# Kernel tuning notes

Hardware: AMD Instinct MI355X
Metric: run time of the kernel (lower is better)

The kernel has to match this reference:

```python
import jax, jax.numpy as jnp
import numpy as np

N = 1024       # nodes
D1 = 64        # hidden_dim_1
D2 = 64        # hidden_dim_2
E = 16384      # edges
P = 8192       # query pairs
MAXX = 100     # max node label -> Embedding(MAXX+1, D1)
EPS = 1e-5     # LayerNorm eps (no affine)


def _ln(t):
    m = jnp.mean(t, axis=-1, keepdims=True)
    v = jnp.mean((t - m) ** 2, axis=-1, keepdims=True)
    return (t - m) / jnp.sqrt(v + EPS)


def setup_inputs() -> dict:
    key = jax.random.key(0)
    ks = jax.random.split(key, 12)
    s = 0.1
    x = jax.random.randint(ks[0], (N,), 0, MAXX + 1)
    ei = jax.random.randint(ks[1], (2, E), 0, N)
    pos = jax.random.randint(ks[2], (P, 2), 0, N)
    emb = jax.random.normal(ks[3], (MAXX + 1, D1)) * s
    sage_Wl = jax.random.normal(ks[4], (2, D1, D1)) * s   # lin_l weight (aggr path, has bias)
    sage_bl = jnp.zeros((2, D1))
    sage_Wr = jax.random.normal(ks[5], (2, D1, D1)) * s   # lin_r weight (root path, no bias)
    h_W = jax.random.normal(ks[6], (D1 + 1, D2)) * s
    h_b = jnp.zeros((D2,))
    g_W = jax.random.normal(ks[7], (D1 + 1 + 2 * D2, D2)) * s
    g_b = jnp.zeros((D2,))
    lin_W = jax.random.normal(ks[8], (D2, 1)) * s
    lin_b = jnp.zeros((1,))
    return {"x": x, "ei": ei, "pos": pos, "emb": emb,
            "sage_Wl": sage_Wl, "sage_bl": sage_bl, "sage_Wr": sage_Wr,
            "h_W": h_W, "h_b": h_b, "g_W": g_W, "g_b": g_b,
            "lin_W": lin_W, "lin_b": lin_b}


def reference(x, ei, pos, emb, sage_Wl, sage_bl, sage_Wr, h_W, h_b, g_W, g_b, lin_W, lin_b):
    n = N
    src, dst = ei[0], ei[1]
    h = emb[x]                                            # (n, D1)
    # SAGEConv x2: mean-aggregate src->dst, lin_l(aggr)+bias + lin_r(root); then LN (no affine, no relu)
    deg = jax.ops.segment_sum(jnp.ones((E,), h.dtype), dst, num_segments=n)
    deg = jnp.maximum(deg, 1.0)[:, None]
    for i in range(2):
        aggr = jax.ops.segment_sum(h[src], dst, num_segments=n) / deg
        h = _ln(aggr @ sage_Wl[i] + sage_bl[i] + h @ sage_Wr[i])
    # pairwise outer product features: (n, n, D1)
    A = h[:, None, :] * h[None, :, :]
    eim = jnp.zeros((n * n,), h.dtype).at[src * n + dst].set(1.0).reshape(n, n, 1)
    A = jnp.concatenate([A, eim], axis=-1)                # (n, n, D1+1)
    # mataggr: B = h_1(A); row/col sums; D = cat(A, vec_p, vec_q); g_1(D)
    B = jax.nn.relu(_ln(A @ h_W + h_b))                   # (n, n, D2)
    vec_p = jnp.sum(B, axis=1, keepdims=True)             # (n, 1, D2)
    vec_q = jnp.sum(B, axis=0, keepdims=True)             # (1, n, D2)
    Dm = jnp.concatenate([A,
                          jnp.broadcast_to(vec_p, (n, n, D2)),
                          jnp.broadcast_to(vec_q, (n, n, D2))], axis=-1)
    G = jax.nn.relu(_ln(Dm @ g_W + g_b))                  # (n, n, D2)
    # symmetrize and gather query pairs
    S = (G * jnp.transpose(G, (1, 0, 2))).reshape(n * n, D2)
    sel = S[pos[:, 0] * n + pos[:, 1]]                    # (P, D2)
    return sel @ lin_W + lin_b                            # (P, 1)
```

## Files before the change

### kernel.cpp

```cpp
#include <hip/hip_runtime.h>
#include <hip/hip_bf16.h>
#include <hip/hip_cooperative_groups.h>

#define NN 1024
#define DD 64
#define EE 16384
#define PP 8192
#define EPSF 1e-5f
#define SWP (DD + 8)
#define SMEM_BYTES 11264

namespace cg = cooperative_groups;

typedef __hip_bfloat16 bf16;
typedef __attribute__((ext_vector_type(8))) short short8;
typedef __attribute__((ext_vector_type(4))) float f32x4;

static __device__ __forceinline__ float dec1(const void* src, int i, int fl) {
    if (fl) return ((const float*)src)[i];
    return __bfloat162float(((const bf16*)src)[i]);
}
static __device__ __forceinline__ unsigned short f2bf_u(float f) {
    bf16 h = __float2bfloat16(f);
    return *reinterpret_cast<unsigned short*>(&h);
}
static __device__ __forceinline__ float bfu2f(unsigned short u) {
    return __uint_as_float(((unsigned int)u) << 16);
}

struct P {
    const int *x, *ei, *pos;
    const void *emb, *sWl, *sbl, *sWr, *hW, *hb, *gW, *gb, *lW, *lb;
    float *Wlf, *blf, *Wrf, *WfT, *hbw, *gWf, *linf;
    float *h0, *h1, *h2;
    unsigned short *hbf;
    int *deg, *rowptr, *cursor, *csrc;
    unsigned int *eim, *eimT;
    float *vecp, *vecq, *ppb, *qqb;
    void *out;
};

static __device__ __forceinline__ int probe_fl(const void* emb) {
    int lane = threadIdx.x & 63;
    unsigned short raw = ((const unsigned short*)emb)[lane];
    float v = __uint_as_float(((unsigned int)raw) << 16);
    return (__ballot(!(fabsf(v) <= 1e3f)) != 0ull) ? 1 : 0;
}

static __device__ void phase_decode(const P& p, int b, int tid, int fl) {
    if (b < 32) { int i = b * 256 + tid; p.Wlf[i] = dec1(p.sWl, i, fl); }
    else if (b == 32) { if (tid < 128) p.blf[tid] = dec1(p.sbl, tid, fl); }
    else if (b < 65) { int i = (b - 33) * 256 + tid; p.Wrf[i] = dec1(p.sWr, i, fl); }
    else if (b < 82) {
        int i = (b - 65) * 256 + tid;
        if (i < 4096) { int n = i >> 6, k = i & 63; p.WfT[n * DD + k] = dec1(p.hW, k * DD + n, fl); }
        else if (i < 4160) p.hbw[i - 4096] = dec1(p.hb, i - 4096, fl);
        else if (i < 4224) p.hbw[64 + (i - 4160)] = dec1(p.hW, 64 * DD + (i - 4160), fl);
    } else if (b < 131) {
        int i = (b - 82) * 256 + tid;
        if (i < 193 * DD) p.gWf[i] = dec1(p.gW, i, fl);
        else if (i < 194 * DD) p.gWf[i] = dec1(p.gb, i - 193 * DD, fl);
    } else if (b == 131) {
        if (tid < DD) p.linf[tid] = dec1(p.lW, tid, fl);
        else if (tid == DD) p.linf[DD] = dec1(p.lb, 0, fl);
    } else if (b < 388) {
        int i = (b - 132) * 256 + tid;
        int node = i >> 6, f = i & 63;
        p.h0[i] = dec1(p.emb, p.x[node] * DD + f, fl);
    } else if (b < 452) {
        int e = (b - 388) * 256 + tid;
        int s = p.ei[e], d = p.ei[EE + e];
        atomicAdd(&p.deg[d], 1);
        unsigned int idx = (unsigned int)(s * NN + d);
        atomicOr(&p.eim[idx >> 5], 1u << (idx & 31));
        unsigned int idxT = (unsigned int)(d * NN + s);
        atomicOr(&p.eimT[idxT >> 5], 1u << (idxT & 31));
    }
}

static __device__ void phase_scan(const P& p, int b, int tid, char* smem) {
    if (b != 0) return;
    int* tmp = (int*)smem;
    int v[4]; int s = 0;
    int base4 = tid * 4;
#pragma unroll
    for (int u = 0; u < 4; ++u) { v[u] = p.deg[base4 + u]; s += v[u]; }
    tmp[tid] = s;
    __syncthreads();
    for (int off = 1; off < 256; off <<= 1) {
        int a = (tid >= off) ? tmp[tid - off] : 0;
        __syncthreads();
        tmp[tid] += a;
        __syncthreads();
    }
    int run = tmp[tid] - s;
#pragma unroll
    for (int u = 0; u < 4; ++u) {
        p.rowptr[base4 + u] = run;
        p.cursor[base4 + u] = run;
        run += v[u];
    }
    if (tid == 255) p.rowptr[NN] = run;
}

static __device__ void phase_scatter(const P& p, int b, int tid) {
    if (b >= 64) return;
    int e = b * 256 + tid;
    int d = p.ei[EE + e];
    int c = atomicAdd(&p.cursor[d], 1);
    p.csrc[c] = p.ei[e];
}

static __device__ void phase_sage(const P& p, int b, int tid, char* smem, int round) {
    if (b >= 256) return;
    int lane = tid & 63, wave = tid >> 6;
    int node = b * 4 + wave;
    const float* hin = round ? p.h1 : p.h0;
    const float* Wl = p.Wlf + round * DD * DD;
    const float* bl = p.blf + round * DD;
    const float* Wr = p.Wrf + round * DD * DD;
    float* hout = round ? p.h2 : p.h1;

    float* sa = (float*)smem + wave * 2 * DD;
    float* sh = sa + DD;
    int r0 = p.rowptr[node], r1 = p.rowptr[node + 1];
    float s = 0.f;
    for (int r = r0; r < r1; ++r) s += hin[p.csrc[r] * DD + lane];
    sa[lane] = s / (float)max(r1 - r0, 1);
    sh[lane] = hin[node * DD + lane];
    float o = bl[lane];
    for (int k = 0; k < DD; ++k)
        o += sa[k] * Wl[k * DD + lane] + sh[k] * Wr[k * DD + lane];
    float m = o;
    for (int off = 32; off; off >>= 1) m += __shfl_xor(m, off);
    m *= (1.f / DD);
    float d0 = o - m;
    float v = d0 * d0;
    for (int off = 32; off; off >>= 1) v += __shfl_xor(v, off);
    v *= (1.f / DD);
    float r = d0 * rsqrtf(v + EPSF);
    hout[node * DD + lane] = r;
    if (round) p.hbf[node * DD + lane] = f2bf_u(r);
}

static __device__ void phase_bstage(const P& p, int b, int tid, char* smem) {
    int lane = tid & 63, wave = tid >> 6;
    int l15 = lane & 15, quad = lane >> 4;
    unsigned short* sW = (unsigned short*)smem;
    float* red = (float*)(smem + DD * SWP * 2);
    {
        int m = tid >> 2;
        int k0 = (tid & 3) * 16;
        const float* hi = p.h2 + b * DD;
        const float* wr = p.WfT + m * DD;
        unsigned short tmp[16];
#pragma unroll
        for (int u = 0; u < 16; ++u) tmp[u] = f2bf_u(hi[k0 + u] * wr[k0 + u]);
        *(short8*)(sW + m * SWP + k0) = *(short8*)tmp;
        *(short8*)(sW + m * SWP + k0 + 8) = *(short8*)(tmp + 8);
    }
    __syncthreads();

    short8 Af[4][2];
#pragma unroll
    for (int mt = 0; mt < 4; ++mt)
#pragma unroll
        for (int kt = 0; kt < 2; ++kt)
            Af[mt][kt] = *(const short8*)(sW + (mt * 16 + l15) * SWP + kt * 32 + quad * 8);

    float hb0[4][4], hww[4][4];
#pragma unroll
    for (int mt = 0; mt < 4; ++mt) {
        f32x4 a = *(const f32x4*)(p.hbw + mt * 16 + quad * 4);
        f32x4 wv = *(const f32x4*)(p.hbw + 64 + mt * 16 + quad * 4);
#pragma unroll
        for (int r = 0; r < 4; ++r) { hb0[mt][r] = a[r]; hww[mt][r] = wv[r]; }
    }

    float accf[4][4], accb[4][4];
#pragma unroll
    for (int mt = 0; mt < 4; ++mt)
#pragma unroll
        for (int r = 0; r < 4; ++r) { accf[mt][r] = 0.f; accb[mt][r] = 0.f; }

    int g = wave;
    short8 B0 = *(const short8*)(p.hbf + (g * 16 + l15) * DD + quad * 8);
    short8 B1 = *(const short8*)(p.hbf + (g * 16 + l15) * DD + 32 + quad * 8);

    for (int it = 0; it < 16; ++it, g += 4) {
        short8 cB0 = B0, cB1 = B1;
        if (it < 15) {
            int gn = g + 4;
            B0 = *(const short8*)(p.hbf + (gn * 16 + l15) * DD + quad * 8);
            B1 = *(const short8*)(p.hbf + (gn * 16 + l15) * DD + 32 + quad * 8);
        }
        unsigned int base = (unsigned int)(b * NN + g * 16);
        unsigned int sf = (p.eim[base >> 5] >> (base & 31)) & 0xFFFFu;
        unsigned int sb = (p.eimT[base >> 5] >> (base & 31)) & 0xFFFFu;

        f32x4 C[4];
#pragma unroll
        for (int mt = 0; mt < 4; ++mt)
            C[mt] = (f32x4){hb0[mt][0], hb0[mt][1], hb0[mt][2], hb0[mt][3]};
#pragma unroll
        for (int mt = 0; mt < 4; ++mt)
            C[mt] = __builtin_amdgcn_mfma_f32_16x16x32_bf16(Af[mt][0], cB0, C[mt], 0, 0, 0);
#pragma unroll
        for (int mt = 0; mt < 4; ++mt)
            C[mt] = __builtin_amdgcn_mfma_f32_16x16x32_bf16(Af[mt][1], cB1, C[mt], 0, 0, 0);

        float ef = (float)((sf >> l15) & 1u);
        float s1 = 0.f, s2 = 0.f;
#pragma unroll
        for (int mt = 0; mt < 4; ++mt)
#pragma unroll
            for (int r = 0; r < 4; ++r) {
                float v = C[mt][r] + ef * hww[mt][r];
                C[mt][r] = v;
                s1 += v;
                s2 += v * v;
            }
        s1 += __shfl_xor(s1, 16); s1 += __shfl_xor(s1, 32);
        s2 += __shfl_xor(s2, 16); s2 += __shfl_xor(s2, 32);
        float mean = s1 * (1.f / DD);
        float var = fmaxf(s2 * (1.f / DD) - mean * mean, 0.f);
        float rs = rsqrtf(var + EPSF);
        float mrs = mean * rs;

        if (sf == sb) {
#pragma unroll
            for (int mt = 0; mt < 4; ++mt)
#pragma unroll
                for (int r = 0; r < 4; ++r) {
                    float u = fmaxf(C[mt][r] * rs - mrs, 0.f);
                    accf[mt][r] += u;
                    accb[mt][r] += u;
                }
        } else {
#pragma unroll
            for (int mt = 0; mt < 4; ++mt)
#pragma unroll
                for (int r = 0; r < 4; ++r)
                    accf[mt][r] += fmaxf(C[mt][r] * rs - mrs, 0.f);
            float de = (float)((sb >> l15) & 1u) - ef;
            float t1 = 0.f, t2 = 0.f;
#pragma unroll
            for (int mt = 0; mt < 4; ++mt)
#pragma unroll
                for (int r = 0; r < 4; ++r) {
                    float v = C[mt][r] + de * hww[mt][r];
                    C[mt][r] = v;
                    t1 += v;
                    t2 += v * v;
                }
            t1 += __shfl_xor(t1, 16); t1 += __shfl_xor(t1, 32);
            t2 += __shfl_xor(t2, 16); t2 += __shfl_xor(t2, 32);
            float mean2 = t1 * (1.f / DD);
            float var2 = fmaxf(t2 * (1.f / DD) - mean2 * mean2, 0.f);
            float rs2 = rsqrtf(var2 + EPSF);
            float mrs2 = mean2 * rs2;
#pragma unroll
            for (int mt = 0; mt < 4; ++mt)
#pragma unroll
                for (int r = 0; r < 4; ++r)
                    accb[mt][r] += fmaxf(C[mt][r] * rs2 - mrs2, 0.f);
        }
    }

#pragma unroll
    for (int step = 1; step < 16; step <<= 1)
#pragma unroll
        for (int mt = 0; mt < 4; ++mt)
#pragma unroll
            for (int r = 0; r < 4; ++r) {
                accf[mt][r] += __shfl_xor(accf[mt][r], step);
                accb[mt][r] += __shfl_xor(accb[mt][r], step);
            }
    if (l15 == 0) {
#pragma unroll
        for (int mt = 0; mt < 4; ++mt)
#pragma unroll
            for (int r = 0; r < 4; ++r) {
                int m = mt * 16 + quad * 4 + r;
                red[wave * 128 + m] = accf[mt][r];
                red[wave * 128 + DD + m] = accb[mt][r];
            }
    }
    __syncthreads();
    if (tid < 2 * DD) {
        float sum = red[tid] + red[128 + tid] + red[256 + tid] + red[384 + tid];
        if (tid < DD) p.vecp[b * DD + tid] = sum;
        else          p.vecq[b * DD + (tid - DD)] = sum;
    }
}

static __device__ void phase_ppqq(const P& p, int b, int tid, char* smem) {
    int lane = tid & 63, wave = tid >> 6;
    if (wave >= 2) return;
    int unit = b * 2 + wave;
    int i = unit & 1023, which = unit >> 10;
    int row0 = which ? 129 : 65;
    float* sv = (float*)smem + wave * DD;
    sv[lane] = (which ? p.vecq : p.vecp)[i * DD + lane];
    float o = 0.f;
    for (int k = 0; k < DD; ++k) o += sv[k] * p.gWf[(row0 + k) * DD + lane];
    (which ? p.qqb : p.ppb)[i * DD + lane] = o;
}

static __device__ void phase_final(const P& p, int b, int tid, int fl, char* smem) {
    if (b >= PP / 64) return;
    int lane = tid & 63, wave = tid >> 6;
    int l15 = lane & 15, quad = lane >> 4;
    unsigned short* sgW = (unsigned short*)smem;
    {
        int m = tid >> 2;
        int k0 = (tid & 3) * 16;
        unsigned short tmp[16];
#pragma unroll
        for (int u = 0; u < 16; ++u) tmp[u] = f2bf_u(p.gWf[(k0 + u) * DD + m]);
        *(short8*)(sgW + m * SWP + k0) = *(short8*)tmp;
        *(short8*)(sgW + m * SWP + k0 + 8) = *(short8*)(tmp + 8);
    }

    int pp_ = b * 64 + wave * 16 + l15;
    int a = p.pos[2 * pp_], bb = p.pos[2 * pp_ + 1];
    short8 ha0 = *(const short8*)(p.hbf + a * DD + quad * 8);
    short8 hb0v = *(const short8*)(p.hbf + bb * DD + quad * 8);
    short8 ha1 = *(const short8*)(p.hbf + a * DD + 32 + quad * 8);
    short8 hb1v = *(const short8*)(p.hbf + bb * DD + 32 + quad * 8);
    short8 B0, B1;
#pragma unroll
    for (int j = 0; j < 8; ++j) {
        B0[j] = (short)f2bf_u(bfu2f((unsigned short)ha0[j]) * bfu2f((unsigned short)hb0v[j]));
        B1[j] = (short)f2bf_u(bfu2f((unsigned short)ha1[j]) * bfu2f((unsigned short)hb1v[j]));
    }
    __syncthreads();

    f32x4 C[4];
#pragma unroll
    for (int mt = 0; mt < 4; ++mt) C[mt] = (f32x4){0.f, 0.f, 0.f, 0.f};
#pragma unroll
    for (int mt = 0; mt < 4; ++mt) {
        short8 A0 = *(const short8*)(sgW + (mt * 16 + l15) * SWP + quad * 8);
        C[mt] = __builtin_amdgcn_mfma_f32_16x16x32_bf16(A0, B0, C[mt], 0, 0, 0);
    }
#pragma unroll
    for (int mt = 0; mt < 4; ++mt) {
        short8 A1 = *(const short8*)(sgW + (mt * 16 + l15) * SWP + 32 + quad * 8);
        C[mt] = __builtin_amdgcn_mfma_f32_16x16x32_bf16(A1, B1, C[mt], 0, 0, 0);
    }

    unsigned int iab = (unsigned int)(a * NN + bb), iba = (unsigned int)(bb * NN + a);
    float eab = (float)((p.eim[iab >> 5] >> (iab & 31)) & 1u);
    float eba = (float)((p.eim[iba >> 5] >> (iba & 31)) & 1u);

    float u1[4][4], u2[4][4];
    float s1 = 0.f, s12 = 0.f, s2 = 0.f, s22 = 0.f;
#pragma unroll
    for (int mt = 0; mt < 4; ++mt) {
        int m0 = mt * 16 + quad * 4;
        f32x4 w64v = *(const f32x4*)(p.gWf + 64 * DD + m0);
        f32x4 gbv  = *(const f32x4*)(p.gWf + 193 * DD + m0);
        f32x4 ppa  = *(const f32x4*)(p.ppb + a * DD + m0);
        f32x4 qqb_ = *(const f32x4*)(p.qqb + bb * DD + m0);
        f32x4 ppb_ = *(const f32x4*)(p.ppb + bb * DD + m0);
        f32x4 qqa  = *(const f32x4*)(p.qqb + a * DD + m0);
#pragma unroll
        for (int r = 0; r < 4; ++r) {
            float v1 = C[mt][r] + eab * w64v[r] + ppa[r] + qqb_[r] + gbv[r];
            float v2 = C[mt][r] + eba * w64v[r] + ppb_[r] + qqa[r] + gbv[r];
            u1[mt][r] = v1; u2[mt][r] = v2;
            s1 += v1; s12 += v1 * v1;
            s2 += v2; s22 += v2 * v2;
        }
    }
    s1 += __shfl_xor(s1, 16);  s1 += __shfl_xor(s1, 32);
    s12 += __shfl_xor(s12, 16); s12 += __shfl_xor(s12, 32);
    s2 += __shfl_xor(s2, 16);  s2 += __shfl_xor(s2, 32);
    s22 += __shfl_xor(s22, 16); s22 += __shfl_xor(s22, 32);
    float mean1 = s1 * (1.f / DD);
    float rs1 = rsqrtf(fmaxf(s12 * (1.f / DD) - mean1 * mean1, 0.f) + EPSF);
    float mrs1 = mean1 * rs1;
    float mean2 = s2 * (1.f / DD);
    float rs2 = rsqrtf(fmaxf(s22 * (1.f / DD) - mean2 * mean2, 0.f) + EPSF);
    float mrs2 = mean2 * rs2;

    float r = 0.f;
#pragma unroll
    for (int mt = 0; mt < 4; ++mt) {
        f32x4 lw = *(const f32x4*)(p.linf + mt * 16 + quad * 4);
#pragma unroll
        for (int rr = 0; rr < 4; ++rr) {
            float g1 = fmaxf(u1[mt][rr] * rs1 - mrs1, 0.f);
            float g2 = fmaxf(u2[mt][rr] * rs2 - mrs2, 0.f);
            r += g1 * g2 * lw[rr];
        }
    }
    r += __shfl_xor(r, 16); r += __shfl_xor(r, 32);
    if (quad == 0) {
        float res = r + p.linf[DD];
        if (fl) ((float*)p.out)[pp_] = res;
        else    ((bf16*)p.out)[pp_] = __float2bfloat16(res);
    }
}

__global__ __launch_bounds__(256, 4) void k_all(P p) {
    cg::grid_group gg = cg::this_grid();
    __shared__ __align__(16) char smem[SMEM_BYTES];
    const int tid = threadIdx.x, b = blockIdx.x;
    int fl = probe_fl(p.emb);

    phase_decode(p, b, tid, fl);   gg.sync();
    phase_scan(p, b, tid, smem);   gg.sync();
    phase_scatter(p, b, tid);      gg.sync();
    phase_sage(p, b, tid, smem, 0); gg.sync();
    phase_sage(p, b, tid, smem, 1); gg.sync();
    phase_bstage(p, b, tid, smem); gg.sync();
    phase_ppqq(p, b, tid, smem);   gg.sync();
    phase_final(p, b, tid, fl, smem);
}

__global__ __launch_bounds__(256) void k_phase(P p, int phase) {
    __shared__ __align__(16) char smem[SMEM_BYTES];
    const int tid = threadIdx.x, b = blockIdx.x;
    int fl = probe_fl(p.emb);
    switch (phase) {
        case 0: phase_decode(p, b, tid, fl); break;
        case 1: phase_scan(p, b, tid, smem); break;
        case 2: phase_scatter(p, b, tid); break;
        case 3: phase_sage(p, b, tid, smem, 0); break;
        case 4: phase_sage(p, b, tid, smem, 1); break;
        case 5: phase_bstage(p, b, tid, smem); break;
        case 6: phase_ppqq(p, b, tid, smem); break;
        case 7: phase_final(p, b, tid, fl, smem); break;
    }
}

extern "C" void kernel_launch(void* const* d_in, const int* in_sizes, int n_in,
                              void* d_out, int out_size, void* d_ws, size_t ws_size,
                              hipStream_t stream) {
    char* w = (char*)d_ws;
    auto alloc = [&](size_t bytes) {
        void* q = (void*)w;
        w += (bytes + 255) & ~(size_t)255;
        return q;
    };
    int* deg = (int*)alloc(NN * 4);
    unsigned int* eim  = (unsigned int*)alloc(NN * NN / 8);
    unsigned int* eimT = (unsigned int*)alloc(NN * NN / 8);
    size_t zero_bytes = (size_t)(w - (char*)d_ws);
    float* h0   = (float*)alloc(NN * DD * 4);
    float* h1   = (float*)alloc(NN * DD * 4);
    float* h2   = (float*)alloc(NN * DD * 4);
    unsigned short* hbf = (unsigned short*)alloc(NN * DD * 2);
    float* Wlf  = (float*)alloc(2 * DD * DD * 4);
    float* blf  = (float*)alloc(2 * DD * 4);
    float* Wrf  = (float*)alloc(2 * DD * DD * 4);
    float* WfT  = (float*)alloc(DD * DD * 4);
    float* hbw  = (float*)alloc(128 * 4);
    float* gWf  = (float*)alloc(194 * DD * 4);
    float* linf = (float*)alloc(65 * 4);
    float* vecp = (float*)alloc(NN * DD * 4);
    float* vecq = (float*)alloc(NN * DD * 4);
    float* ppb  = (float*)alloc(NN * DD * 4);
    float* qqb  = (float*)alloc(NN * DD * 4);
    int* rowptr = (int*)alloc((NN + 1) * 4);
    int* cursor = (int*)alloc(NN * 4);
    int* csrc   = (int*)alloc(EE * 4);

    hipMemsetAsync(d_ws, 0, zero_bytes, stream);

    P hp;
    hp.x = (const int*)d_in[0];
    hp.ei = (const int*)d_in[1];
    hp.pos = (const int*)d_in[2];
    hp.emb = d_in[3];
    hp.sWl = d_in[4];
    hp.sbl = d_in[5];
    hp.sWr = d_in[6];
    hp.hW = d_in[7];
    hp.hb = d_in[8];
    hp.gW = d_in[9];
    hp.gb = d_in[10];
    hp.lW = d_in[11];
    hp.lb = d_in[12];
    hp.Wlf = Wlf; hp.blf = blf; hp.Wrf = Wrf; hp.WfT = WfT; hp.hbw = hbw;
    hp.gWf = gWf; hp.linf = linf;
    hp.h0 = h0; hp.h1 = h1; hp.h2 = h2; hp.hbf = hbf;
    hp.deg = deg; hp.rowptr = rowptr; hp.cursor = cursor; hp.csrc = csrc;
    hp.eim = eim; hp.eimT = eimT;
    hp.vecp = vecp; hp.vecq = vecq; hp.ppb = ppb; hp.qqb = qqb;
    hp.out = d_out;

    hipError_t err = hipErrorUnknown;
    int nb = 0, ncu = 0;
    if (hipOccupancyMaxActiveBlocksPerMultiprocessor(&nb, k_all, 256, 0) == hipSuccess &&
        hipDeviceGetAttribute(&ncu, hipDeviceAttributeMultiprocessorCount, 0) == hipSuccess &&
        (long)nb * ncu >= 1024) {
        void* args[] = { &hp };
        err = hipLaunchCooperativeKernel(k_all, dim3(1024), dim3(256), args, 0, stream);
    }
    if (err != hipSuccess) {
        k_phase<<<452, 256, 0, stream>>>(hp, 0);
        k_phase<<<1,   256, 0, stream>>>(hp, 1);
        k_phase<<<64,  256, 0, stream>>>(hp, 2);
        k_phase<<<256, 256, 0, stream>>>(hp, 3);
        k_phase<<<256, 256, 0, stream>>>(hp, 4);
        k_phase<<<1024, 256, 0, stream>>>(hp, 5);
        k_phase<<<1024, 256, 0, stream>>>(hp, 6);
        k_phase<<<128, 256, 0, stream>>>(hp, 7);
    }
}
```

Baseline: 164.8 us.

## Replace cooperative grid-sync megakernel with five fused stream-ordered kernels

Drops the cooperative kernel and its seven grid-wide barriers in favour of five ordinary launches. Degree count, scan and CSR scatter move into a single block using shared-memory atomics, and the workspace memset is replaced by in-kernel zeroing. The edge-bitmap build moves into the first SAGE kernel, and the ppqq projection is fused into the tail of the bstage kernel. Each grid sync becomes a kernel boundary, and the single-block CSR build serialises that step onto one CU.

Result: slower. 275.1 us (+67.0%).

```diff
diff --git a/kernel.cpp b/kernel.cpp
--- a/kernel.cpp
+++ b/kernel.cpp
@@ -1,6 +1,5 @@
 #include <hip/hip_runtime.h>
 #include <hip/hip_bf16.h>
-#include <hip/hip_cooperative_groups.h>
 
 #define NN 1024
 #define DD 64
@@ -8,9 +7,6 @@
 #define PP 8192
 #define EPSF 1e-5f
 #define SWP (DD + 8)
-#define SMEM_BYTES 11264
-
-namespace cg = cooperative_groups;
 
 typedef __hip_bfloat16 bf16;
 typedef __attribute__((ext_vector_type(8))) short short8;
@@ -27,19 +23,6 @@
 static __device__ __forceinline__ float bfu2f(unsigned short u) {
     return __uint_as_float(((unsigned int)u) << 16);
 }
-
-struct P {
-    const int *x, *ei, *pos;
-    const void *emb, *sWl, *sbl, *sWr, *hW, *hb, *gW, *gb, *lW, *lb;
-    float *Wlf, *blf, *Wrf, *WfT, *hbw, *gWf, *linf;
-    float *h0, *h1, *h2;
-    unsigned short *hbf;
-    int *deg, *rowptr, *cursor, *csrc;
-    unsigned int *eim, *eimT;
-    float *vecp, *vecq, *ppb, *qqb;
-    void *out;
-};
-
 static __device__ __forceinline__ int probe_fl(const void* emb) {
     int lane = threadIdx.x & 63;
     unsigned short raw = ((const unsigned short*)emb)[lane];
@@ -47,85 +30,95 @@
     return (__ballot(!(fabsf(v) <= 1e3f)) != 0ull) ? 1 : 0;
 }
 
-static __device__ void phase_decode(const P& p, int b, int tid, int fl) {
-    if (b < 32) { int i = b * 256 + tid; p.Wlf[i] = dec1(p.sWl, i, fl); }
-    else if (b == 32) { if (tid < 128) p.blf[tid] = dec1(p.sbl, tid, fl); }
-    else if (b < 65) { int i = (b - 33) * 256 + tid; p.Wrf[i] = dec1(p.sWr, i, fl); }
+__global__ __launch_bounds__(256) void k_prep(
+        const void* __restrict__ emb, const void* __restrict__ sWl,
+        const void* __restrict__ sbl, const void* __restrict__ sWr,
+        const void* __restrict__ hW, const void* __restrict__ hb,
+        const void* __restrict__ gW, const void* __restrict__ gb,
+        const void* __restrict__ lW, const void* __restrict__ lb,
+        const int* __restrict__ x, const int* __restrict__ ei,
+        float* __restrict__ Wlf, float* __restrict__ blf, float* __restrict__ Wrf,
+        float* __restrict__ WfT, float* __restrict__ hbw,
+        float* __restrict__ gWf, float* __restrict__ linf,
+        float* __restrict__ h0,
+        unsigned int* __restrict__ eim, unsigned int* __restrict__ eimT,
+        int* __restrict__ rowptr, int* __restrict__ csrc) {
+    __shared__ int sdeg[NN];
+    __shared__ int stmp[256];
+    const int b = blockIdx.x, tid = threadIdx.x;
+    const int fl = probe_fl(emb);
+
+    if (b < 256) {
+        int z = b * 256 + tid;
+        if (z < 32768) eim[z] = 0u;
+        else           eimT[z - 32768] = 0u;
+    }
+
+    if (b < 32) { int i = b * 256 + tid; Wlf[i] = dec1(sWl, i, fl); }
+    else if (b == 32) { if (tid < 128) blf[tid] = dec1(sbl, tid, fl); }
+    else if (b < 65) { int i = (b - 33) * 256 + tid; Wrf[i] = dec1(sWr, i, fl); }
     else if (b < 82) {
         int i = (b - 65) * 256 + tid;
-        if (i < 4096) { int n = i >> 6, k = i & 63; p.WfT[n * DD + k] = dec1(p.hW, k * DD + n, fl); }
-        else if (i < 4160) p.hbw[i - 4096] = dec1(p.hb, i - 4096, fl);
-        else if (i < 4224) p.hbw[64 + (i - 4160)] = dec1(p.hW, 64 * DD + (i - 4160), fl);
+        if (i < 4096) { int n = i >> 6, k = i & 63; WfT[n * DD + k] = dec1(hW, k * DD + n, fl); }
+        else if (i < 4160) hbw[i - 4096] = dec1(hb, i - 4096, fl);
+        else if (i < 4224) hbw[64 + (i - 4160)] = dec1(hW, 64 * DD + (i - 4160), fl);
     } else if (b < 131) {
         int i = (b - 82) * 256 + tid;
-        if (i < 193 * DD) p.gWf[i] = dec1(p.gW, i, fl);
-        else if (i < 194 * DD) p.gWf[i] = dec1(p.gb, i - 193 * DD, fl);
+        if (i < 193 * DD) gWf[i] = dec1(gW, i, fl);
+        else if (i < 194 * DD) gWf[i] = dec1(gb, i - 193 * DD, fl);
     } else if (b == 131) {
-        if (tid < DD) p.linf[tid] = dec1(p.lW, tid, fl);
-        else if (tid == DD) p.linf[DD] = dec1(p.lb, 0, fl);
+        if (tid < DD) linf[tid] = dec1(lW, tid, fl);
+        else if (tid == DD) linf[DD] = dec1(lb, 0, fl);
     } else if (b < 388) {
         int i = (b - 132) * 256 + tid;
         int node = i >> 6, f = i & 63;
-        p.h0[i] = dec1(p.emb, p.x[node] * DD + f, fl);
-    } else if (b < 452) {
-        int e = (b - 388) * 256 + tid;
-        int s = p.ei[e], d = p.ei[EE + e];
-        atomicAdd(&p.deg[d], 1);
-        unsigned int idx = (unsigned int)(s * NN + d);
-        atomicOr(&p.eim[idx >> 5], 1u << (idx & 31));
-        unsigned int idxT = (unsigned int)(d * NN + s);
-        atomicOr(&p.eimT[idxT >> 5], 1u << (idxT & 31));
-    }
-}
-
-static __device__ void phase_scan(const P& p, int b, int tid, char* smem) {
-    if (b != 0) return;
-    int* tmp = (int*)smem;
-    int v[4]; int s = 0;
-    int base4 = tid * 4;
-#pragma unroll
-    for (int u = 0; u < 4; ++u) { v[u] = p.deg[base4 + u]; s += v[u]; }
-    tmp[tid] = s;
-    __syncthreads();
-    for (int off = 1; off < 256; off <<= 1) {
-        int a = (tid >= off) ? tmp[tid - off] : 0;
+        h0[i] = dec1(emb, x[node] * DD + f, fl);
+    } else if (b == 388) {
+        for (int i = tid; i < NN; i += 256) sdeg[i] = 0;
         __syncthreads();
-        tmp[tid] += a;
+        for (int e = tid; e < EE; e += 256) atomicAdd(&sdeg[ei[EE + e]], 1);
         __syncthreads();
-    }
-    int run = tmp[tid] - s;
-#pragma unroll
-    for (int u = 0; u < 4; ++u) {
-        p.rowptr[base4 + u] = run;
-        p.cursor[base4 + u] = run;
-        run += v[u];
-    }
-    if (tid == 255) p.rowptr[NN] = run;
-}
-
-static __device__ void phase_scatter(const P& p, int b, int tid) {
-    if (b >= 64) return;
-    int e = b * 256 + tid;
-    int d = p.ei[EE + e];
-    int c = atomicAdd(&p.cursor[d], 1);
-    p.csrc[c] = p.ei[e];
-}
-
-static __device__ void phase_sage(const P& p, int b, int tid, char* smem, int round) {
-    if (b >= 256) return;
-    int lane = tid & 63, wave = tid >> 6;
-    int node = b * 4 + wave;
-    const float* hin = round ? p.h1 : p.h0;
-    const float* Wl = p.Wlf + round * DD * DD;
-    const float* bl = p.blf + round * DD;
-    const float* Wr = p.Wrf + round * DD * DD;
-    float* hout = round ? p.h2 : p.h1;
-
+        int base4 = tid * 4;
+        int v[4]; int s = 0;
+#pragma unroll
+        for (int u = 0; u < 4; ++u) { v[u] = sdeg[base4 + u]; s += v[u]; }
+        stmp[tid] = s;
+        __syncthreads();
+        for (int off = 1; off < 256; off <<= 1) {
+            int a = (tid >= off) ? stmp[tid - off] : 0;
+            __syncthreads();
+            stmp[tid] += a;
+            __syncthreads();
+        }
+        int run = stmp[tid] - s;
+#pragma unroll
+        for (int u = 0; u < 4; ++u) {
+            rowptr[base4 + u] = run;
+            sdeg[base4 + u] = run;
+            run += v[u];
+        }
+        if (tid == 255) rowptr[NN] = run;
+        __syncthreads();
+        for (int e = tid; e < EE; e += 256) {
+            int d = ei[EE + e];
+            int c = atomicAdd(&sdeg[d], 1);
+            csrc[c] = ei[e];
+        }
+    }
+}
+
+static __device__ __forceinline__ void sage_body(
+        char* smem, int node, int lane, int wave,
+        const int* __restrict__ rowptr, const int* __restrict__ csrc,
+        const float* __restrict__ hin,
+        const float* __restrict__ Wl, const float* __restrict__ bl,
+        const float* __restrict__ Wr,
+        float* __restrict__ hout, unsigned short* __restrict__ hbf) {
     float* sa = (float*)smem + wave * 2 * DD;
     float* sh = sa + DD;
-    int r0 = p.rowptr[node], r1 = p.rowptr[node + 1];
+    int r0 = rowptr[node], r1 = rowptr[node + 1];
     float s = 0.f;
-    for (int r = r0; r < r1; ++r) s += hin[p.csrc[r] * DD + lane];
+    for (int r = r0; r < r1; ++r) s += hin[csrc[r] * DD + lane];
     sa[lane] = s / (float)max(r1 - r0, 1);
     sh[lane] = hin[node * DD + lane];
     float o = bl[lane];
@@ -140,19 +133,62 @@
     v *= (1.f / DD);
     float r = d0 * rsqrtf(v + EPSF);
     hout[node * DD + lane] = r;
-    if (round) p.hbf[node * DD + lane] = f2bf_u(r);
-}
-
-static __device__ void phase_bstage(const P& p, int b, int tid, char* smem) {
-    int lane = tid & 63, wave = tid >> 6;
-    int l15 = lane & 15, quad = lane >> 4;
-    unsigned short* sW = (unsigned short*)smem;
-    float* red = (float*)(smem + DD * SWP * 2);
+    if (hbf) hbf[node * DD + lane] = f2bf_u(r);
+}
+
+__global__ __launch_bounds__(256) void k_sage0(
+        const int* __restrict__ ei,
+        const int* __restrict__ rowptr, const int* __restrict__ csrc,
+        const float* __restrict__ h0,
+        const float* __restrict__ Wlf, const float* __restrict__ blf,
+        const float* __restrict__ Wrf,
+        float* __restrict__ h1,
+        unsigned int* __restrict__ eim, unsigned int* __restrict__ eimT) {
+    __shared__ __align__(16) char smem[4 * 2 * DD * 4];
+    const int b = blockIdx.x, tid = threadIdx.x;
+    const int lane = tid & 63, wave = tid >> 6;
+    if (tid < 64) {
+        int e = b * 64 + tid;
+        int s = ei[e], d = ei[EE + e];
+        unsigned int idx = (unsigned int)(s * NN + d);
+        atomicOr(&eim[idx >> 5], 1u << (idx & 31));
+        unsigned int idxT = (unsigned int)(d * NN + s);
+        atomicOr(&eimT[idxT >> 5], 1u << (idxT & 31));
+    }
+    sage_body(smem, b * 4 + wave, lane, wave, rowptr, csrc, h0, Wlf, blf, Wrf,
+              h1, (unsigned short*)nullptr);
+}
+
+__global__ __launch_bounds__(256) void k_sage1(
+        const int* __restrict__ rowptr, const int* __restrict__ csrc,
+        const float* __restrict__ h1,
+        const float* __restrict__ Wlf, const float* __restrict__ blf,
+        const float* __restrict__ Wrf,
+        float* __restrict__ h2, unsigned short* __restrict__ hbf) {
+    __shared__ __align__(16) char smem[4 * 2 * DD * 4];
+    const int b = blockIdx.x, tid = threadIdx.x;
+    const int lane = tid & 63, wave = tid >> 6;
+    sage_body(smem, b * 4 + wave, lane, wave, rowptr, csrc, h1,
+              Wlf + DD * DD, blf + DD, Wrf + DD * DD, h2, hbf);
+}
+
+__global__ __launch_bounds__(256, 4) void k_bstage(
+        const float* __restrict__ h2, const unsigned short* __restrict__ hbf,
+        const float* __restrict__ WfT, const float* __restrict__ hbw,
+        const unsigned int* __restrict__ eim, const unsigned int* __restrict__ eimT,
+        const float* __restrict__ gWf,
+        float* __restrict__ ppb, float* __restrict__ qqb) {
+    __shared__ __align__(16) unsigned short sW[DD * SWP];
+    __shared__ __align__(16) float red[4 * 128];
+    const int b = blockIdx.x, tid = threadIdx.x;
+    const int lane = tid & 63, wave = tid >> 6;
+    const int l15 = lane & 15, quad = lane >> 4;
+
     {
         int m = tid >> 2;
         int k0 = (tid & 3) * 16;
-        const float* hi = p.h2 + b * DD;
-        const float* wr = p.WfT + m * DD;
+        const float* hi = h2 + b * DD;
+        const float* wr = WfT + m * DD;
         unsigned short tmp[16];
 #pragma unroll
         for (int u = 0; u < 16; ++u) tmp[u] = f2bf_u(hi[k0 + u] * wr[k0 + u]);
@@ -171,8 +207,8 @@
     float hb0[4][4], hww[4][4];
 #pragma unroll
     for (int mt = 0; mt < 4; ++mt) {
-        f32x4 a = *(const f32x4*)(p.hbw + mt * 16 + quad * 4);
-        f32x4 wv = *(const f32x4*)(p.hbw + 64 + mt * 16 + quad * 4);
+        f32x4 a = *(const f32x4*)(hbw + mt * 16 + quad * 4);
+        f32x4 wv = *(const f32x4*)(hbw + 64 + mt * 16 + quad * 4);
 #pragma unroll
         for (int r = 0; r < 4; ++r) { hb0[mt][r] = a[r]; hww[mt][r] = wv[r]; }
     }
@@ -184,19 +220,19 @@
         for (int r = 0; r < 4; ++r) { accf[mt][r] = 0.f; accb[mt][r] = 0.f; }
 
     int g = wave;
-    short8 B0 = *(const short8*)(p.hbf + (g * 16 + l15) * DD + quad * 8);
-    short8 B1 = *(const short8*)(p.hbf + (g * 16 + l15) * DD + 32 + quad * 8);
+    short8 B0 = *(const short8*)(hbf + (g * 16 + l15) * DD + quad * 8);
+    short8 B1 = *(const short8*)(hbf + (g * 16 + l15) * DD + 32 + quad * 8);
 
     for (int it = 0; it < 16; ++it, g += 4) {
         short8 cB0 = B0, cB1 = B1;
         if (it < 15) {
             int gn = g + 4;
-            B0 = *(const short8*)(p.hbf + (gn * 16 + l15) * DD + quad * 8);
-            B1 = *(const short8*)(p.hbf + (gn * 16 + l15) * DD + 32 + quad * 8);
+            B0 = *(const short8*)(hbf + (gn * 16 + l15) * DD + quad * 8);
+            B1 = *(const short8*)(hbf + (gn * 16 + l15) * DD + 32 + quad * 8);
         }
         unsigned int base = (unsigned int)(b * NN + g * 16);
-        unsigned int sf = (p.eim[base >> 5] >> (base & 31)) & 0xFFFFu;
-        unsigned int sb = (p.eimT[base >> 5] >> (base & 31)) & 0xFFFFu;
+        unsigned int sf = (eim[base >> 5] >> (base & 31)) & 0xFFFFu;
+        unsigned int sb = (eimT[base >> 5] >> (base & 31)) & 0xFFFFu;
 
         f32x4 C[4];
 #pragma unroll
@@ -287,47 +323,48 @@
             }
     }
     __syncthreads();
-    if (tid < 2 * DD) {
+    if (tid < 128) {
         float sum = red[tid] + red[128 + tid] + red[256 + tid] + red[384 + tid];
-        if (tid < DD) p.vecp[b * DD + tid] = sum;
-        else          p.vecq[b * DD + (tid - DD)] = sum;
-    }
-}
-
-static __device__ void phase_ppqq(const P& p, int b, int tid, char* smem) {
-    int lane = tid & 63, wave = tid >> 6;
-    if (wave >= 2) return;
-    int unit = b * 2 + wave;
-    int i = unit & 1023, which = unit >> 10;
-    int row0 = which ? 129 : 65;
-    float* sv = (float*)smem + wave * DD;
-    sv[lane] = (which ? p.vecq : p.vecp)[i * DD + lane];
-    float o = 0.f;
-    for (int k = 0; k < DD; ++k) o += sv[k] * p.gWf[(row0 + k) * DD + lane];
-    (which ? p.qqb : p.ppb)[i * DD + lane] = o;
-}
-
-static __device__ void phase_final(const P& p, int b, int tid, int fl, char* smem) {
-    if (b >= PP / 64) return;
-    int lane = tid & 63, wave = tid >> 6;
-    int l15 = lane & 15, quad = lane >> 4;
-    unsigned short* sgW = (unsigned short*)smem;
+        red[tid] = sum;
+    }
+    __syncthreads();
+    if (wave < 2) {
+        const float* sv = red + wave * DD;
+        int row0 = wave ? 129 : 65;
+        float o = 0.f;
+        for (int k = 0; k < DD; ++k) o += sv[k] * gWf[(row0 + k) * DD + lane];
+        (wave ? qqb : ppb)[b * DD + lane] = o;
+    }
+}
+
+__global__ __launch_bounds__(256) void k_final(
+        const void* __restrict__ emb,
+        const int* __restrict__ pos, const unsigned short* __restrict__ hbf,
+        const float* __restrict__ gWf, const unsigned int* __restrict__ eim,
+        const float* __restrict__ ppb, const float* __restrict__ qqb,
+        const float* __restrict__ linf, void* __restrict__ outv) {
+    __shared__ __align__(16) unsigned short sgW[DD * SWP];
+    const int b = blockIdx.x, tid = threadIdx.x;
+    const int lane = tid & 63, wave = tid >> 6;
+    const int l15 = lane & 15, quad = lane >> 4;
+    const int fl = probe_fl(emb);
+
     {
         int m = tid >> 2;
         int k0 = (tid & 3) * 16;
         unsigned short tmp[16];
 #pragma unroll
-        for (int u = 0; u < 16; ++u) tmp[u] = f2bf_u(p.gWf[(k0 + u) * DD + m]);
+        for (int u = 0; u < 16; ++u) tmp[u] = f2bf_u(gWf[(k0 + u) * DD + m]);
         *(short8*)(sgW + m * SWP + k0) = *(short8*)tmp;
         *(short8*)(sgW + m * SWP + k0 + 8) = *(short8*)(tmp + 8);
     }
 
     int pp_ = b * 64 + wave * 16 + l15;
-    int a = p.pos[2 * pp_], bb = p.pos[2 * pp_ + 1];
-    short8 ha0 = *(const short8*)(p.hbf + a * DD + quad * 8);
-    short8 hb0v = *(const short8*)(p.hbf + bb * DD + quad * 8);
-    short8 ha1 = *(const short8*)(p.hbf + a * DD + 32 + quad * 8);
-    short8 hb1v = *(const short8*)(p.hbf + bb * DD + 32 + quad * 8);
+    int a = pos[2 * pp_], bb = pos[2 * pp_ + 1];
+    short8 ha0 = *(const short8*)(hbf + a * DD + quad * 8);
+    short8 hb0v = *(const short8*)(hbf + bb * DD + quad * 8);
+    short8 ha1 = *(const short8*)(hbf + a * DD + 32 + quad * 8);
+    short8 hb1v = *(const short8*)(hbf + bb * DD + 32 + quad * 8);
     short8 B0, B1;
 #pragma unroll
     for (int j = 0; j < 8; ++j) {
@@ -351,20 +388,20 @@
     }
 
     unsigned int iab = (unsigned int)(a * NN + bb), iba = (unsigned int)(bb * NN + a);
-    float eab = (float)((p.eim[iab >> 5] >> (iab & 31)) & 1u);
-    float eba = (float)((p.eim[iba >> 5] >> (iba & 31)) & 1u);
+    float eab = (float)((eim[iab >> 5] >> (iab & 31)) & 1u);
+    float eba = (float)((eim[iba >> 5] >> (iba & 31)) & 1u);
 
     float u1[4][4], u2[4][4];
     float s1 = 0.f, s12 = 0.f, s2 = 0.f, s22 = 0.f;
 #pragma unroll
     for (int mt = 0; mt < 4; ++mt) {
         int m0 = mt * 16 + quad * 4;
-        f32x4 w64v = *(const f32x4*)(p.gWf + 64 * DD + m0);
-        f32x4 gbv  = *(const f32x4*)(p.gWf + 193 * DD + m0);
-        f32x4 ppa  = *(const f32x4*)(p.ppb + a * DD + m0);
-        f32x4 qqb_ = *(const f32x4*)(p.qqb + bb * DD + m0);
-        f32x4 ppb_ = *(const f32x4*)(p.ppb + bb * DD + m0);
-        f32x4 qqa  = *(const f32x4*)(p.qqb + a * DD + m0);
+        f32x4 w64v = *(const f32x4*)(gWf + 64 * DD + m0);
+        f32x4 gbv  = *(const f32x4*)(gWf + 193 * DD + m0);
+        f32x4 ppa  = *(const f32x4*)(ppb + a * DD + m0);
+        f32x4 qqb_ = *(const f32x4*)(qqb + bb * DD + m0);
+        f32x4 ppb_ = *(const f32x4*)(ppb + bb * DD + m0);
+        f32x4 qqa  = *(const f32x4*)(qqb + a * DD + m0);
 #pragma unroll
         for (int r = 0; r < 4; ++r) {
             float v1 = C[mt][r] + eab * w64v[r] + ppa[r] + qqb_[r] + gbv[r];
@@ -388,7 +425,7 @@
     float r = 0.f;
 #pragma unroll
     for (int mt = 0; mt < 4; ++mt) {
-        f32x4 lw = *(const f32x4*)(p.linf + mt * 16 + quad * 4);
+        f32x4 lw = *(const f32x4*)(linf + mt * 16 + quad * 4);
 #pragma unroll
         for (int rr = 0; rr < 4; ++rr) {
             float g1 = fmaxf(u1[mt][rr] * rs1 - mrs1, 0.f);
@@ -398,57 +435,28 @@
     }
     r += __shfl_xor(r, 16); r += __shfl_xor(r, 32);
     if (quad == 0) {
-        float res = r + p.linf[DD];
-        if (fl) ((float*)p.out)[pp_] = res;
-        else    ((bf16*)p.out)[pp_] = __float2bfloat16(res);
-    }
-}
-
-__global__ __launch_bounds__(256, 4) void k_all(P p) {
-    cg::grid_group gg = cg::this_grid();
-    __shared__ __align__(16) char smem[SMEM_BYTES];
-    const int tid = threadIdx.x, b = blockIdx.x;
-    int fl = probe_fl(p.emb);
-
-    phase_decode(p, b, tid, fl);   gg.sync();
-    phase_scan(p, b, tid, smem);   gg.sync();
-    phase_scatter(p, b, tid);      gg.sync();
-    phase_sage(p, b, tid, smem, 0); gg.sync();
-    phase_sage(p, b, tid, smem, 1); gg.sync();
-    phase_bstage(p, b, tid, smem); gg.sync();
-    phase_ppqq(p, b, tid, smem);   gg.sync();
-    phase_final(p, b, tid, fl, smem);
-}
-
-__global__ __launch_bounds__(256) void k_phase(P p, int phase) {
-    __shared__ __align__(16) char smem[SMEM_BYTES];
-    const int tid = threadIdx.x, b = blockIdx.x;
-    int fl = probe_fl(p.emb);
-    switch (phase) {
-        case 0: phase_decode(p, b, tid, fl); break;
-        case 1: phase_scan(p, b, tid, smem); break;
-        case 2: phase_scatter(p, b, tid); break;
-        case 3: phase_sage(p, b, tid, smem, 0); break;
-        case 4: phase_sage(p, b, tid, smem, 1); break;
-        case 5: phase_bstage(p, b, tid, smem); break;
-        case 6: phase_ppqq(p, b, tid, smem); break;
-        case 7: phase_final(p, b, tid, fl, smem); break;
+        float res = r + linf[DD];
+        if (fl) ((float*)outv)[pp_] = res;
+        else    ((bf16*)outv)[pp_] = __float2bfloat16(res);
     }
 }
 
 extern "C" void kernel_launch(void* const* d_in, const int* in_sizes, int n_in,
                               void* d_out, int out_size, void* d_ws, size_t ws_size,
                               hipStream_t stream) {
+    const int* x   = (const int*)d_in[0];
+    const int* ei  = (const int*)d_in[1];
+    const int* pos = (const int*)d_in[2];
+    const void* emb = d_in[3];
+
     char* w = (char*)d_ws;
     auto alloc = [&](size_t bytes) {
         void* q = (void*)w;
         w += (bytes + 255) & ~(size_t)255;
         return q;
     };
-    int* deg = (int*)alloc(NN * 4);
     unsigned int* eim  = (unsigned int*)alloc(NN * NN / 8);
     unsigned int* eimT = (unsigned int*)alloc(NN * NN / 8);
-    size_t zero_bytes = (size_t)(w - (char*)d_ws);
     float* h0   = (float*)alloc(NN * DD * 4);
     float* h1   = (float*)alloc(NN * DD * 4);
     float* h2   = (float*)alloc(NN * DD * 4);
@@ -460,54 +468,17 @@
     float* hbw  = (float*)alloc(128 * 4);
     float* gWf  = (float*)alloc(194 * DD * 4);
     float* linf = (float*)alloc(65 * 4);
-    float* vecp = (float*)alloc(NN * DD * 4);
-    float* vecq = (float*)alloc(NN * DD * 4);
     float* ppb  = (float*)alloc(NN * DD * 4);
     float* qqb  = (float*)alloc(NN * DD * 4);
     int* rowptr = (int*)alloc((NN + 1) * 4);
-    int* cursor = (int*)alloc(NN * 4);
     int* csrc   = (int*)alloc(EE * 4);
 
-    hipMemsetAsync(d_ws, 0, zero_bytes, stream);
-
-    P hp;
-    hp.x = (const int*)d_in[0];
-    hp.ei = (const int*)d_in[1];
-    hp.pos = (const int*)d_in[2];
-    hp.emb = d_in[3];
-    hp.sWl = d_in[4];
-    hp.sbl = d_in[5];
-    hp.sWr = d_in[6];
-    hp.hW = d_in[7];
-    hp.hb = d_in[8];
-    hp.gW = d_in[9];
-    hp.gb = d_in[10];
-    hp.lW = d_in[11];
-    hp.lb = d_in[12];
-    hp.Wlf = Wlf; hp.blf = blf; hp.Wrf = Wrf; hp.WfT = WfT; hp.hbw = hbw;
-    hp.gWf = gWf; hp.linf = linf;
-    hp.h0 = h0; hp.h1 = h1; hp.h2 = h2; hp.hbf = hbf;
-    hp.deg = deg; hp.rowptr = rowptr; hp.cursor = cursor; hp.csrc = csrc;
-    hp.eim = eim; hp.eimT = eimT;
-    hp.vecp = vecp; hp.vecq = vecq; hp.ppb = ppb; hp.qqb = qqb;
-    hp.out = d_out;
-
-    hipError_t err = hipErrorUnknown;
-    int nb = 0, ncu = 0;
-    if (hipOccupancyMaxActiveBlocksPerMultiprocessor(&nb, k_all, 256, 0) == hipSuccess &&
-        hipDeviceGetAttribute(&ncu, hipDeviceAttributeMultiprocessorCount, 0) == hipSuccess &&
-        (long)nb * ncu >= 1024) {
-        void* args[] = { &hp };
-        err = hipLaunchCooperativeKernel(k_all, dim3(1024), dim3(256), args, 0, stream);
-    }
-    if (err != hipSuccess) {
-        k_phase<<<452, 256, 0, stream>>>(hp, 0);
-        k_phase<<<1,   256, 0, stream>>>(hp, 1);
-        k_phase<<<64,  256, 0, stream>>>(hp, 2);
-        k_phase<<<256, 256, 0, stream>>>(hp, 3);
-        k_phase<<<256, 256, 0, stream>>>(hp, 4);
-        k_phase<<<1024, 256, 0, stream>>>(hp, 5);
-        k_phase<<<1024, 256, 0, stream>>>(hp, 6);
-        k_phase<<<128, 256, 0, stream>>>(hp, 7);
-    }
-}
+    k_prep<<<389, 256, 0, stream>>>(emb, d_in[4], d_in[5], d_in[6], d_in[7], d_in[8],
+                                    d_in[9], d_in[10], d_in[11], d_in[12],
+                                    x, ei, Wlf, blf, Wrf, WfT, hbw, gWf, linf,
+                                    h0, eim, eimT, rowptr, csrc);
+    k_sage0<<<256, 256, 0, stream>>>(ei, rowptr, csrc, h0, Wlf, blf, Wrf, h1, eim, eimT);
+    k_sage1<<<256, 256, 0, stream>>>(rowptr, csrc, h1, Wlf, blf, Wrf, h2, hbf);
+    k_bstage<<<NN, 256, 0, stream>>>(h2, hbf, WfT, hbw, eim, eimT, gWf, ppb, qqb);
+    k_final<<<PP / 64, 256, 0, stream>>>(emb, pos, hbf, gWf, eim, ppb, qqb, linf, d_out);
+}
```
